# Optimization experiments

Measured on AMD Instinct MI355X. Metric: run time of the kernel, lower is better.

## Reference

```python
import jax, jax.numpy as jnp
import numpy as np

B, S, F, FFN = 8, 1024, 1024, 4096
F2 = FFN // 2          # NMF 'N' dim
R = 64                 # hamburger MD_R default
STEPS = 6              # number_of_iterations (TRAIN_STEPS == EVAL_STEPS)
EPS = 1e-6             # NMF2D denominator eps
LN_EPS = 1e-5


def setup_inputs() -> dict:
    key = jax.random.key(0)
    ks = jax.random.split(key, 6)
    x = jax.random.normal(ks[0], (B, S, F), jnp.float32)
    Wu = jax.random.normal(ks[1], (FFN, F), jnp.float32) / np.sqrt(F).astype(np.float32)
    bu = jnp.zeros((FFN,), jnp.float32)
    gamma = jnp.ones((F2,), jnp.float32)
    beta = jnp.zeros((F2,), jnp.float32)
    Wv = jax.random.normal(ks[2], (F, F2), jnp.float32) / np.sqrt(F2).astype(np.float32)
    bv = jnp.zeros((F,), jnp.float32)
    # NMF2D._build_bases: rand then F.normalize(dim=1) i.e. L2 over D(=seq) axis
    bases = jax.random.uniform(ks[3], (S, R), jnp.float32)
    bases = bases / jnp.linalg.norm(bases, axis=0, keepdims=True)
    return dict(x=x, Wu=Wu, bu=bu, gamma=gamma, beta=beta, Wv=Wv, bv=bv, bases=bases)


def _nmf_local_inference(xm, bas):
    # xm: (B, D, N) nonnegative, bas: (B, D, R)
    coef = jax.nn.softmax(jnp.einsum('bdn,bdr->bnr', xm, bas), axis=-1)  # inv_t = 1 for NMF2D

    def step(carry, _):
        bas, coef = carry
        # multiplicative update for coef (B, N, R)
        numer = jnp.einsum('bdn,bdr->bnr', xm, bas)
        denom = coef @ jnp.einsum('bdr,bds->brs', bas, bas)
        coef = coef * numer / (denom + EPS)
        # multiplicative update for bases (B, D, R)
        numer = jnp.einsum('bdn,bnr->bdr', xm, coef)
        denom = bas @ jnp.einsum('bnr,bns->brs', coef, coef)
        bas = bas * numer / (denom + EPS)
        return (bas, coef), None

    (bas, coef), _ = jax.lax.scan(step, (bas, coef), None, length=STEPS)
    return bas, coef


def reference(x, Wu, bu, gamma, beta, Wv, bv, bases):
    # gated MLP front: GELU(U(x)), chunk, ReLU(LN(z2))
    h = jax.nn.gelu(x @ Wu.T + bu, approximate=False)          # (B, S, FFN)
    z1, z2 = jnp.split(h, 2, axis=-1)                           # (B, S, F2) each
    mu = jnp.mean(z2, axis=-1, keepdims=True)
    var = jnp.mean((z2 - mu) ** 2, axis=-1, keepdims=True)
    z2 = (z2 - mu) / jnp.sqrt(var + LN_EPS) * gamma + beta
    z2 = jax.nn.relu(z2)

    # NMF2D: x viewed as (B, D=S, N=F2); bases buffer repeated over batch
    xm = z2                                                     # (B, D, N)
    bas0 = jnp.tile(bases[None], (B, 1, 1))                     # (B, D, R)
    # iterative solver runs under torch.no_grad in the original
    bas, coef = _nmf_local_inference(jax.lax.stop_gradient(xm), bas0)
    bas = jax.lax.stop_gradient(bas)
    coef = jax.lax.stop_gradient(coef)

    # compute_coef: one coef update WITH gradient through xm
    numer = jnp.einsum('bdn,bdr->bnr', xm, bas)
    denom = coef @ jnp.einsum('bdr,bds->brs', bas, bas)
    coef = coef * numer / (denom + EPS)

    z2r = jnp.einsum('bdr,bnr->bdn', bas, coef)                 # (B, S, F2) reconstruction

    out = (z1 * z2r) @ Wv.T + bv                                # (B, S, F)
    return out
```

## Files before the change

### kernel.cpp

```cpp
#include <hip/hip_runtime.h>
#include <math.h>

#define B_ 8
#define S_ 1024
#define F_ 1024
#define FFN_ 4096
#define F2_ 2048
#define R_ 64
#define NSTEPS 6
#define EPS_ 1e-6f
#define LN_EPS_ 1e-5f

typedef unsigned short u16;
typedef __attribute__((ext_vector_type(8))) short bf16x8;
typedef __attribute__((ext_vector_type(8))) unsigned short u16x8;
typedef __attribute__((ext_vector_type(4))) float f32x4;

__device__ __forceinline__ u16 f2bf(float f) {
    union { float f; unsigned int u; } c; c.f = f;
    unsigned int r = c.u + 0x7FFF + ((c.u >> 16) & 1);
    return (u16)(r >> 16);
}
__device__ __forceinline__ float bf2f(u16 u) {
    union { unsigned int u; float f; } c; c.u = ((unsigned int)u) << 16;
    return c.f;
}

__global__ __launch_bounds__(256) void k_cvt_bf16(const float* __restrict__ in,
        u16* __restrict__ out, int n8) {
    int i = blockIdx.x * 256 + threadIdx.x;
    if (i >= n8) return;
    const float4* p = (const float4*)in + (size_t)i * 2;
    float4 a = p[0], b = p[1];
    u16x8 o;
    o[0] = f2bf(a.x); o[1] = f2bf(a.y); o[2] = f2bf(a.z); o[3] = f2bf(a.w);
    o[4] = f2bf(b.x); o[5] = f2bf(b.y); o[6] = f2bf(b.z); o[7] = f2bf(b.w);
    *((u16x8*)out + i) = o;
}

template<int KD, int NOUT, bool GELUSPLIT>
__global__ __launch_bounds__(256) void k_mfma_bt(
        const u16* __restrict__ A, const u16* __restrict__ Bw,
        const float* __restrict__ bias,
        u16* __restrict__ obf, float* __restrict__ of1) {
    __shared__ u16 As[128 * 32];
    __shared__ u16 Bs[128 * 32];
    const int bm = blockIdx.x * 128;
    const int bn = blockIdx.y * 128;
    const int tid = threadIdx.x;
    const int wid = tid >> 6, lane = tid & 63;
    const int wr = wid >> 1, wc = wid & 1;
    const int lrow = lane & 15, lk = (lane >> 4) * 8;
    const int srow = lane >> 2, scol = (lane & 3) * 8;

    f32x4 acc[4][4] = {};

    const u16* Ag = A + (size_t)(bm + wid * 32) * KD;
    const u16* Bg = Bw + (size_t)(bn + wid * 32) * KD;

    for (int k0 = 0; k0 < KD; k0 += 32) {
        #pragma unroll
        for (int c = 0; c < 2; c++) {
            const u16* ga = Ag + (size_t)(c * 16 + srow) * KD + k0 + scol;
            u16* la = &As[(wid * 32 + c * 16) * 32];
            __builtin_amdgcn_global_load_lds(
                (const __attribute__((address_space(1))) void*)ga,
                (__attribute__((address_space(3))) void*)la, 16, 0, 0);
            const u16* gb = Bg + (size_t)(c * 16 + srow) * KD + k0 + scol;
            u16* lb = &Bs[(wid * 32 + c * 16) * 32];
            __builtin_amdgcn_global_load_lds(
                (const __attribute__((address_space(1))) void*)gb,
                (__attribute__((address_space(3))) void*)lb, 16, 0, 0);
        }
        __syncthreads();
        bf16x8 af[4], bfv[4];
        #pragma unroll
        for (int m = 0; m < 4; m++)
            af[m] = *(const bf16x8*)&As[(wr * 64 + m * 16 + lrow) * 32 + lk];
        #pragma unroll
        for (int n = 0; n < 4; n++)
            bfv[n] = *(const bf16x8*)&Bs[(wc * 64 + n * 16 + lrow) * 32 + lk];
        #pragma unroll
        for (int m = 0; m < 4; m++)
            #pragma unroll
            for (int n = 0; n < 4; n++)
                acc[m][n] = __builtin_amdgcn_mfma_f32_16x16x32_bf16(
                        af[m], bfv[n], acc[m][n], 0, 0, 0);
        __syncthreads();
    }

    const int crow = (lane >> 4) * 4;
    const int ccol = lane & 15;
    #pragma unroll
    for (int m = 0; m < 4; m++) {
        const int row = bm + wr * 64 + m * 16 + crow;
        #pragma unroll
        for (int n = 0; n < 4; n++) {
            const int col = bn + wc * 64 + n * 16 + ccol;
            const float bz = bias[col];
            #pragma unroll
            for (int r = 0; r < 4; r++) {
                float v = acc[m][n][r] + bz;
                if (GELUSPLIT) {
                    float g = 0.5f * v * (1.0f + erff(v * 0.7071067811865476f));
                    if (col < F2_) obf[(size_t)(row + r) * F2_ + col] = f2bf(g);
                    else           of1[(size_t)(row + r) * F2_ + (col - F2_)] = g;
                } else {
                    of1[(size_t)(row + r) * NOUT + col] = v;
                }
            }
        }
    }
}

template<int BM, int KD, int KCH, int M>
__global__ __launch_bounds__(256) void k_nmf_bt(
        const u16* __restrict__ A, const u16* __restrict__ Bw,
        float* __restrict__ outp) {
    __shared__ u16 As[BM * 32];
    __shared__ u16 Bs[64 * 32];
    constexpr int MR = BM / 32;
    const int bm = blockIdx.x * BM;
    const int ks = blockIdx.y;
    const int b  = blockIdx.z;
    const u16* Ab = A + (size_t)b * M * KD;
    const u16* Bb = Bw + (size_t)b * 64 * KD;
    const int tid = threadIdx.x;
    const int wid = tid >> 6, lane = tid & 63;
    const int wr = wid >> 1, wc = wid & 1;
    const int lrow = lane & 15, lk = (lane >> 4) * 8;
    const int srow = lane >> 2, scol = (lane & 3) * 8;

    f32x4 acc[MR][2] = {};
    const int kbeg = ks * (KD / KCH), kend = kbeg + KD / KCH;

    for (int k0 = kbeg; k0 < kend; k0 += 32) {
        #pragma unroll
        for (int c = 0; c < BM / 64; c++) {
            const int rowb = c * 64 + wid * 16;
            const u16* ga = Ab + (size_t)(bm + rowb + srow) * KD + k0 + scol;
            u16* la = &As[rowb * 32];
            __builtin_amdgcn_global_load_lds(
                (const __attribute__((address_space(1))) void*)ga,
                (__attribute__((address_space(3))) void*)la, 16, 0, 0);
        }
        {
            const int rowb = wid * 16;
            const u16* gb = Bb + (size_t)(rowb + srow) * KD + k0 + scol;
            u16* lb = &Bs[rowb * 32];
            __builtin_amdgcn_global_load_lds(
                (const __attribute__((address_space(1))) void*)gb,
                (__attribute__((address_space(3))) void*)lb, 16, 0, 0);
        }
        __syncthreads();
        bf16x8 af[MR], bf2[2];
        #pragma unroll
        for (int m = 0; m < MR; m++)
            af[m] = *(const bf16x8*)&As[(wr * (BM / 2) + m * 16 + lrow) * 32 + lk];
        #pragma unroll
        for (int n = 0; n < 2; n++)
            bf2[n] = *(const bf16x8*)&Bs[(wc * 32 + n * 16 + lrow) * 32 + lk];
        #pragma unroll
        for (int m = 0; m < MR; m++)
            #pragma unroll
            for (int n = 0; n < 2; n++)
                acc[m][n] = __builtin_amdgcn_mfma_f32_16x16x32_bf16(
                        af[m], bf2[n], acc[m][n], 0, 0, 0);
        __syncthreads();
    }

    const int crow = (lane >> 4) * 4;
    const int ccol = lane & 15;
    float* ob = outp + ((size_t)(ks * B_ + b) * M) * 64;
    #pragma unroll
    for (int m = 0; m < MR; m++) {
        const int row = bm + wr * (BM / 2) + m * 16 + crow;
        #pragma unroll
        for (int n = 0; n < 2; n++) {
            const int col = wc * 32 + n * 16 + ccol;
            #pragma unroll
            for (int r = 0; r < 4; r++)
                ob[(size_t)(row + r) * 64 + col] = acc[m][n][r];
        }
    }
}

__global__ __launch_bounds__(256) void k_ln_relu(const float* __restrict__ z2f,
        u16* __restrict__ xm_bf,
        const float* __restrict__ gamma, const float* __restrict__ beta) {
    const int row = blockIdx.x;
    const float* p = z2f + (size_t)row * F2_;
    const int i0 = threadIdx.x * 8;
    float4 a = *(const float4*)(p + i0);
    float4 b = *(const float4*)(p + i0 + 4);
    float v[8] = { a.x, a.y, a.z, a.w, b.x, b.y, b.z, b.w };
    float s = 0.f, sq = 0.f;
    #pragma unroll
    for (int j = 0; j < 8; j++) { s += v[j]; sq += v[j] * v[j]; }
    __shared__ float red0[4], red1[4];
    #pragma unroll
    for (int off = 32; off > 0; off >>= 1) {
        s  += __shfl_down(s, off);
        sq += __shfl_down(sq, off);
    }
    const int wid = threadIdx.x >> 6, lane = threadIdx.x & 63;
    if (lane == 0) { red0[wid] = s; red1[wid] = sq; }
    __syncthreads();
    if (threadIdx.x == 0) {
        float S = red0[0] + red0[1] + red0[2] + red0[3];
        float SQ = red1[0] + red1[1] + red1[2] + red1[3];
        float mu = S * (1.0f / F2_);
        float var = SQ * (1.0f / F2_) - mu * mu;
        red0[0] = mu;
        red1[0] = rsqrtf(var + LN_EPS_);
    }
    __syncthreads();
    const float mu = red0[0], inv = red1[0];
    u16x8 o;
    #pragma unroll
    for (int j = 0; j < 8; j++) {
        float w = (v[j] - mu) * inv * gamma[i0 + j] + beta[i0 + j];
        o[j] = f2bf(w > 0.f ? w : 0.f);
    }
    *(u16x8*)&xm_bf[(size_t)row * F2_ + i0] = o;
}

__global__ __launch_bounds__(256) void k_transpose_bf(const u16* __restrict__ in,
        u16* __restrict__ outp) {
    __shared__ u16 s[64][72];
    const int n0 = blockIdx.x * 64, d0 = blockIdx.y * 64, b = blockIdx.z;
    const u16* ib = in + (size_t)b * S_ * F2_;
    u16* ob = outp + (size_t)b * S_ * F2_;
    const int t = threadIdx.x;
    const int rr = t >> 3, cc = (t & 7) * 8;
    #pragma unroll
    for (int p = 0; p < 2; p++) {
        const int r = rr + p * 32;
        u16x8 v = *(const u16x8*)&ib[(size_t)(d0 + r) * F2_ + n0 + cc];
        #pragma unroll
        for (int j = 0; j < 8; j++) s[r][cc + j] = v[j];
    }
    __syncthreads();
    #pragma unroll
    for (int p = 0; p < 2; p++) {
        const int nr = rr + p * 32;
        u16x8 o;
        #pragma unroll
        for (int j = 0; j < 8; j++) o[j] = s[cc + j][nr];
        *(u16x8*)&ob[(size_t)(n0 + nr) * S_ + d0 + cc] = o;
    }
}

__global__ __launch_bounds__(256) void k_init_bases(const float* __restrict__ bases,
        float* __restrict__ bas, u16* __restrict__ basT) {
    const int i = blockIdx.x * 256 + threadIdx.x;
    const float v = bases[i];
    const int d = i >> 6, r = i & 63;
    const u16 vb = f2bf(v);
    #pragma unroll
    for (int b = 0; b < B_; b++) {
        bas[(size_t)b * S_ * R_ + i] = v;
        basT[(size_t)b * S_ * R_ + (size_t)r * S_ + d] = vb;
    }
}

__global__ __launch_bounds__(256) void k_softmax_coef(const float* __restrict__ ncp,
        float* __restrict__ coef, u16* __restrict__ coefT) {
    const size_t row = (size_t)blockIdx.x * 4 + (threadIdx.x >> 6);
    const int r = threadIdx.x & 63;
    const size_t CH = (size_t)B_ * F2_ * R_;
    float v = ncp[row * R_ + r] + ncp[CH + row * R_ + r];
    float m = v;
    #pragma unroll
    for (int off = 32; off > 0; off >>= 1) m = fmaxf(m, __shfl_xor(m, off));
    const float e = expf(v - m);
    float ssum = e;
    #pragma unroll
    for (int off = 32; off > 0; off >>= 1) ssum += __shfl_xor(ssum, off);
    const float cv = e / ssum;
    coef[row * R_ + r] = cv;
    const int b = (int)(row >> 11), n = (int)(row & 2047);
    coefT[((size_t)b * 64 + r) * F2_ + n] = f2bf(cv);
}

__global__ __launch_bounds__(256) void k_ata_part(const float* __restrict__ A,
        float* __restrict__ Gp, int K) {
    const int ks = blockIdx.x;
    const int b  = blockIdx.y;
    const int chunk = K >> 4;
    const float* Ab = A + ((size_t)b * K + (size_t)ks * chunk) * R_;
    __shared__ float As[16][68];
    const int tid = threadIdx.x, tx = tid & 15, ty = tid >> 4;
    float acc[4][4] = {};
    for (int k0 = 0; k0 < chunk; k0 += 16) {
        const int rr = tid & 63, q = tid >> 6;
        #pragma unroll
        for (int i = 0; i < 4; i++) {
            const int kk = q * 4 + i;
            As[kk][rr] = Ab[(size_t)(k0 + kk) * R_ + rr];
        }
        __syncthreads();
        #pragma unroll
        for (int kk = 0; kk < 16; kk++) {
            float a[4], bb[4];
            #pragma unroll
            for (int i = 0; i < 4; i++) a[i] = As[kk][ty * 4 + i];
            #pragma unroll
            for (int j = 0; j < 4; j++) bb[j] = As[kk][tx * 4 + j];
            #pragma unroll
            for (int i = 0; i < 4; i++)
                #pragma unroll
                for (int j = 0; j < 4; j++)
                    acc[i][j] = fmaf(a[i], bb[j], acc[i][j]);
        }
        __syncthreads();
    }
    #pragma unroll
    for (int i = 0; i < 4; i++)
        #pragma unroll
        for (int j = 0; j < 4; j++)
            Gp[(((size_t)b * 16 + ks) * R_ + ty * 4 + i) * R_ + tx * 4 + j] = acc[i][j];
}

__global__ __launch_bounds__(256) void k_ata_reduce(const float* __restrict__ Gp,
        float* __restrict__ G) {
    const int idx = blockIdx.x * 256 + threadIdx.x;
    const int b = idx >> 12, rs = idx & 4095;
    float s = 0.f;
    #pragma unroll
    for (int ks = 0; ks < 16; ks++) s += Gp[((size_t)b * 16 + ks) * 4096 + rs];
    G[idx] = s;
}

__global__ __launch_bounds__(256) void k_mult_update(float* __restrict__ M_,
        const float* __restrict__ numer_p, const float* __restrict__ G,
        int NR, size_t CH, u16* __restrict__ Tout, int TK) {
    const int b = blockIdx.y;
    const int row = blockIdx.x * 4 + (threadIdx.x >> 6);
    const int r = threadIdx.x & 63;
    __shared__ float Gs[64][68];
    __shared__ float Ms[4][64];
    const float* Gb = G + (size_t)b * R_ * R_;
    for (int i = threadIdx.x; i < 64 * 64; i += 256) Gs[i >> 6][i & 63] = Gb[i];
    const size_t base = ((size_t)b * NR + row) * R_;
    Ms[threadIdx.x >> 6][r] = M_[base + r];
    __syncthreads();
    float acc = 0.f;
    const int lrow = threadIdx.x >> 6;
    #pragma unroll
    for (int s = 0; s < 64; s++) acc = fmaf(Ms[lrow][s], Gs[s][r], acc);
    const float num = numer_p[base + r] + numer_p[CH + base + r];
    const float nv = Ms[lrow][r] * num / (acc + EPS_);
    M_[base + r] = nv;
    Tout[((size_t)b * 64 + r) * TK + row] = f2bf(nv);
}

__global__ __launch_bounds__(256) void k_recon_prod(const float* __restrict__ bas,
        const float* __restrict__ coef, u16* __restrict__ z1_bf) {
    const int d0 = blockIdx.x * 64;
    const int n0 = blockIdx.y * 64;
    const int b  = blockIdx.z;
    __shared__ float BasS[64][65], CoefS[64][65];
    const int tid = threadIdx.x, tx = tid & 15, ty = tid >> 4;
    {
        const int rr = tid & 63, q = tid >> 6;
        #pragma unroll
        for (int i = 0; i < 16; i++) {
            const int rowi = q * 16 + i;
            BasS[rowi][rr]  = bas[((size_t)b * S_ + d0 + rowi) * R_ + rr];
            CoefS[rowi][rr] = coef[((size_t)b * F2_ + n0 + rowi) * R_ + rr];
        }
    }
    __syncthreads();
    float acc[4][4] = {};
    #pragma unroll 8
    for (int r = 0; r < 64; r++) {
        float a[4], bb[4];
        #pragma unroll
        for (int i = 0; i < 4; i++) a[i] = BasS[ty * 4 + i][r];
        #pragma unroll
        for (int j = 0; j < 4; j++) bb[j] = CoefS[tx * 4 + j][r];
        #pragma unroll
        for (int i = 0; i < 4; i++)
            #pragma unroll
            for (int j = 0; j < 4; j++)
                acc[i][j] = fmaf(a[i], bb[j], acc[i][j]);
    }
    #pragma unroll
    for (int i = 0; i < 4; i++) {
        const size_t m = (size_t)b * S_ + d0 + ty * 4 + i;
        const size_t idx = m * F2_ + n0 + tx * 4;
        ushort4 zi = *(const ushort4*)&z1_bf[idx];
        ushort4 o;
        o.x = f2bf(bf2f(zi.x) * acc[i][0]);
        o.y = f2bf(bf2f(zi.y) * acc[i][1]);
        o.z = f2bf(bf2f(zi.z) * acc[i][2]);
        o.w = f2bf(bf2f(zi.w) * acc[i][3]);
        *(ushort4*)&z1_bf[idx] = o;
    }
}

extern "C" void kernel_launch(void* const* d_in, const int* in_sizes, int n_in,
                              void* d_out, int out_size, void* d_ws, size_t ws_size,
                              hipStream_t stream) {
    const float* x     = (const float*)d_in[0];
    const float* Wu    = (const float*)d_in[1];
    const float* bu    = (const float*)d_in[2];
    const float* gamma = (const float*)d_in[3];
    const float* beta  = (const float*)d_in[4];
    const float* Wv    = (const float*)d_in[5];
    const float* bv    = (const float*)d_in[6];
    const float* bases = (const float*)d_in[7];
    float* out = (float*)d_out;

    float* ws = (float*)d_ws;
    const size_t Z   = (size_t)B_ * S_ * F2_;
    const size_t NCR = (size_t)B_ * F2_ * R_;
    const size_t NBR = (size_t)B_ * S_ * R_;

    float* z2f    = ws;
    u16*   xmT_bf = (u16*)z2f;
    float* Gp     = z2f + Z / 2;
    float* G      = Gp + (size_t)16 * B_ * R_ * R_;
    float* p1 = z2f + Z;
    u16*   z1_bf  = (u16*)p1;
    float* p2 = p1 + Z / 2;
    u16*   xm_bf  = (u16*)p2;
    u16*   x_bf   = (u16*)p2;
    float* p3 = p2 + Z / 2;
    float* ncp    = p3;
    u16*   Wu_bf  = (u16*)p3;
    float* p4 = p3 + 2 * NCR;
    float* nbp    = p4;
    float* p5 = p4 + 2 * NBR;
    float* bas    = p5;
    float* p6 = p5 + NBR;
    u16*   basT_bf = (u16*)p6;
    float* p7 = p6 + NBR / 2;
    float* coef   = p7;
    u16*   Wv_bf  = (u16*)p7;
    float* p8 = p7 + NCR;
    u16*   coefT_bf = (u16*)p8;

    k_cvt_bf16<<<dim3(4096), 256, 0, stream>>>(x,  x_bf,  (int)((size_t)B_ * S_ * F_ / 8));
    k_cvt_bf16<<<dim3(2048), 256, 0, stream>>>(Wu, Wu_bf, (int)((size_t)FFN_ * F_ / 8));

    k_mfma_bt<F_, F2_, true><<<dim3(64, 32), 256, 0, stream>>>(x_bf, Wu_bf, bu, z1_bf, z2f);
    k_ln_relu<<<dim3(8192), 256, 0, stream>>>(z2f, xm_bf, gamma, beta);
    k_transpose_bf<<<dim3(32, 16, B_), 256, 0, stream>>>(xm_bf, xmT_bf);
    k_init_bases<<<dim3(256), 256, 0, stream>>>(bases, bas, basT_bf);

    k_nmf_bt<128, S_, 2, F2_><<<dim3(16, 2, B_), 256, 0, stream>>>(xmT_bf, basT_bf, ncp);
    k_softmax_coef<<<dim3(4096), 256, 0, stream>>>(ncp, coef, coefT_bf);

    for (int it = 0; it < NSTEPS; it++) {
        k_nmf_bt<128, S_, 2, F2_><<<dim3(16, 2, B_), 256, 0, stream>>>(xmT_bf, basT_bf, ncp);
        k_ata_part<<<dim3(16, B_), 256, 0, stream>>>(bas, Gp, S_);
        k_ata_reduce<<<dim3(128), 256, 0, stream>>>(Gp, G);
        k_mult_update<<<dim3(512, B_), 256, 0, stream>>>(coef, ncp, G, F2_, NCR, coefT_bf, F2_);
        k_nmf_bt<64, F2_, 2, S_><<<dim3(16, 2, B_), 256, 0, stream>>>(xm_bf, coefT_bf, nbp);
        k_ata_part<<<dim3(16, B_), 256, 0, stream>>>(coef, Gp, F2_);
        k_ata_reduce<<<dim3(128), 256, 0, stream>>>(Gp, G);
        k_mult_update<<<dim3(256, B_), 256, 0, stream>>>(bas, nbp, G, S_, NBR, basT_bf, S_);
    }

    k_nmf_bt<128, S_, 2, F2_><<<dim3(16, 2, B_), 256, 0, stream>>>(xmT_bf, basT_bf, ncp);
    k_ata_part<<<dim3(16, B_), 256, 0, stream>>>(bas, Gp, S_);
    k_ata_reduce<<<dim3(128), 256, 0, stream>>>(Gp, G);
    k_mult_update<<<dim3(512, B_), 256, 0, stream>>>(coef, ncp, G, F2_, NCR, coefT_bf, F2_);

    k_recon_prod<<<dim3(16, 32, B_), 256, 0, stream>>>(bas, coef, z1_bf);

    k_cvt_bf16<<<dim3(1024), 256, 0, stream>>>(Wv, Wv_bf, (int)((size_t)F_ * F2_ / 8));
    k_mfma_bt<F2_, F_, false><<<dim3(64, 8), 256, 0, stream>>>(z1_bf, Wv_bf, bv, nullptr, out);
}
```

Before: 812.3 us.

## Fuse Gram computation into NMF numerator kernel and store z2 as bf16

The separate two-kernel Gram computation (partial plus reduce) is folded into the NMF numerator GEMM launch as extra blocks, each computing a 64x16 slice of the Gram matrix directly. This removes two launches per update and the partial-sum round trip. The first iteration is peeled so the initial numerator launch can be reused by the first coef update. z2 is now written as bf16 instead of fp32 to halve the write and read traffic into LayerNorm, at some cost in LN statistic precision. The extra Gram blocks each scan the full K dimension serially, so they may become the tail of the launch.

```diff
diff --git a/kernel.cpp b/kernel.cpp
--- a/kernel.cpp
+++ b/kernel.cpp
@@ -42,7 +42,7 @@
 __global__ __launch_bounds__(256) void k_mfma_bt(
         const u16* __restrict__ A, const u16* __restrict__ Bw,
         const float* __restrict__ bias,
-        u16* __restrict__ obf, float* __restrict__ of1) {
+        u16* __restrict__ obf, u16* __restrict__ obf2, float* __restrict__ of1) {
     __shared__ u16 As[128 * 32];
     __shared__ u16 Bs[128 * 32];
     const int bm = blockIdx.x * 128;
@@ -104,7 +104,7 @@
                 if (GELUSPLIT) {
                     float g = 0.5f * v * (1.0f + erff(v * 0.7071067811865476f));
                     if (col < F2_) obf[(size_t)(row + r) * F2_ + col] = f2bf(g);
-                    else           of1[(size_t)(row + r) * F2_ + (col - F2_)] = g;
+                    else           obf2[(size_t)(row + r) * F2_ + (col - F2_)] = f2bf(g);
                 } else {
                     of1[(size_t)(row + r) * NOUT + col] = v;
                 }
@@ -113,87 +113,120 @@
     }
 }
 
-template<int BM, int KD, int KCH, int M>
-__global__ __launch_bounds__(256) void k_nmf_bt(
+template<int BM, int KD, int M, int AK>
+__global__ __launch_bounds__(256) void k_numer_gram(
         const u16* __restrict__ A, const u16* __restrict__ Bw,
-        float* __restrict__ outp) {
+        float* __restrict__ outp,
+        const float* __restrict__ Afp, float* __restrict__ G) {
     __shared__ u16 As[BM * 32];
     __shared__ u16 Bs[64 * 32];
-    constexpr int MR = BM / 32;
-    const int bm = blockIdx.x * BM;
-    const int ks = blockIdx.y;
-    const int b  = blockIdx.z;
-    const u16* Ab = A + (size_t)b * M * KD;
-    const u16* Bb = Bw + (size_t)b * 64 * KD;
+    __shared__ float Agr[16][65];
     const int tid = threadIdx.x;
-    const int wid = tid >> 6, lane = tid & 63;
-    const int wr = wid >> 1, wc = wid & 1;
-    const int lrow = lane & 15, lk = (lane >> 4) * 8;
-    const int srow = lane >> 2, scol = (lane & 3) * 8;
-
-    f32x4 acc[MR][2] = {};
-    const int kbeg = ks * (KD / KCH), kend = kbeg + KD / KCH;
-
-    for (int k0 = kbeg; k0 < kend; k0 += 32) {
-        #pragma unroll
-        for (int c = 0; c < BM / 64; c++) {
-            const int rowb = c * 64 + wid * 16;
-            const u16* ga = Ab + (size_t)(bm + rowb + srow) * KD + k0 + scol;
-            u16* la = &As[rowb * 32];
-            __builtin_amdgcn_global_load_lds(
-                (const __attribute__((address_space(1))) void*)ga,
-                (__attribute__((address_space(3))) void*)la, 16, 0, 0);
-        }
-        {
-            const int rowb = wid * 16;
-            const u16* gb = Bb + (size_t)(rowb + srow) * KD + k0 + scol;
-            u16* lb = &Bs[rowb * 32];
-            __builtin_amdgcn_global_load_lds(
-                (const __attribute__((address_space(1))) void*)gb,
-                (__attribute__((address_space(3))) void*)lb, 16, 0, 0);
-        }
-        __syncthreads();
-        bf16x8 af[MR], bf2[2];
-        #pragma unroll
-        for (int m = 0; m < MR; m++)
-            af[m] = *(const bf16x8*)&As[(wr * (BM / 2) + m * 16 + lrow) * 32 + lk];
-        #pragma unroll
-        for (int n = 0; n < 2; n++)
-            bf2[n] = *(const bf16x8*)&Bs[(wc * 32 + n * 16 + lrow) * 32 + lk];
-        #pragma unroll
-        for (int m = 0; m < MR; m++)
+    const int b = blockIdx.z;
+
+    if (blockIdx.x < 16) {
+        constexpr int MR = BM / 32;
+        const int bm = blockIdx.x * BM;
+        const int ks = blockIdx.y;
+        const u16* Ab = A + (size_t)b * M * KD;
+        const u16* Bb = Bw + (size_t)b * 64 * KD;
+        const int wid = tid >> 6, lane = tid & 63;
+        const int wr = wid >> 1, wc = wid & 1;
+        const int lrow = lane & 15, lk = (lane >> 4) * 8;
+        const int srow = lane >> 2, scol = (lane & 3) * 8;
+
+        f32x4 acc[MR][2] = {};
+        const int kbeg = ks * (KD / 2), kend = kbeg + KD / 2;
+
+        for (int k0 = kbeg; k0 < kend; k0 += 32) {
+            #pragma unroll
+            for (int c = 0; c < BM / 64; c++) {
+                const int rowb = c * 64 + wid * 16;
+                const u16* ga = Ab + (size_t)(bm + rowb + srow) * KD + k0 + scol;
+                u16* la = &As[rowb * 32];
+                __builtin_amdgcn_global_load_lds(
+                    (const __attribute__((address_space(1))) void*)ga,
+                    (__attribute__((address_space(3))) void*)la, 16, 0, 0);
+            }
+            {
+                const int rowb = wid * 16;
+                const u16* gb = Bb + (size_t)(rowb + srow) * KD + k0 + scol;
+                u16* lb = &Bs[rowb * 32];
+                __builtin_amdgcn_global_load_lds(
+                    (const __attribute__((address_space(1))) void*)gb,
+                    (__attribute__((address_space(3))) void*)lb, 16, 0, 0);
+            }
+            __syncthreads();
+            bf16x8 af[MR], bf2[2];
+            #pragma unroll
+            for (int m = 0; m < MR; m++)
+                af[m] = *(const bf16x8*)&As[(wr * (BM / 2) + m * 16 + lrow) * 32 + lk];
             #pragma unroll
             for (int n = 0; n < 2; n++)
-                acc[m][n] = __builtin_amdgcn_mfma_f32_16x16x32_bf16(
-                        af[m], bf2[n], acc[m][n], 0, 0, 0);
-        __syncthreads();
-    }
-
-    const int crow = (lane >> 4) * 4;
-    const int ccol = lane & 15;
-    float* ob = outp + ((size_t)(ks * B_ + b) * M) * 64;
-    #pragma unroll
-    for (int m = 0; m < MR; m++) {
-        const int row = bm + wr * (BM / 2) + m * 16 + crow;
-        #pragma unroll
-        for (int n = 0; n < 2; n++) {
-            const int col = wc * 32 + n * 16 + ccol;
-            #pragma unroll
-            for (int r = 0; r < 4; r++)
-                ob[(size_t)(row + r) * 64 + col] = acc[m][n][r];
-        }
-    }
-}
-
-__global__ __launch_bounds__(256) void k_ln_relu(const float* __restrict__ z2f,
+                bf2[n] = *(const bf16x8*)&Bs[(wc * 32 + n * 16 + lrow) * 32 + lk];
+            #pragma unroll
+            for (int m = 0; m < MR; m++)
+                #pragma unroll
+                for (int n = 0; n < 2; n++)
+                    acc[m][n] = __builtin_amdgcn_mfma_f32_16x16x32_bf16(
+                            af[m], bf2[n], acc[m][n], 0, 0, 0);
+            __syncthreads();
+        }
+
+        const int crow = (lane >> 4) * 4;
+        const int ccol = lane & 15;
+        float* ob = outp + ((size_t)(ks * B_ + b) * M) * 64;
+        #pragma unroll
+        for (int m = 0; m < MR; m++) {
+            const int row = bm + wr * (BM / 2) + m * 16 + crow;
+            #pragma unroll
+            for (int n = 0; n < 2; n++) {
+                const int col = wc * 32 + n * 16 + ccol;
+                #pragma unroll
+                for (int r = 0; r < 4; r++)
+                    ob[(size_t)(row + r) * 64 + col] = acc[m][n][r];
+            }
+        }
+    } else {
+        const int schunk = (blockIdx.x - 16) * 2 + blockIdx.y;
+        const int s0 = schunk * 16;
+        const float* Ab = Afp + (size_t)b * AK * 64;
+        const int r = tid & 63;
+        const int sg = tid >> 6;
+        float acc[4] = {};
+        for (int k0 = 0; k0 < AK; k0 += 16) {
+            #pragma unroll
+            for (int i = 0; i < 4; i++) {
+                const int idx = tid + i * 256;
+                Agr[idx >> 6][idx & 63] = Ab[(size_t)(k0 + (idx >> 6)) * 64 + (idx & 63)];
+            }
+            __syncthreads();
+            #pragma unroll
+            for (int kk = 0; kk < 16; kk++) {
+                const float ar = Agr[kk][r];
+                #pragma unroll
+                for (int j = 0; j < 4; j++)
+                    acc[j] = fmaf(ar, Agr[kk][s0 + sg * 4 + j], acc[j]);
+            }
+            __syncthreads();
+        }
+        float* Gb = G + (size_t)b * R_ * R_;
+        #pragma unroll
+        for (int j = 0; j < 4; j++)
+            Gb[(size_t)r * R_ + s0 + sg * 4 + j] = acc[j];
+    }
+}
+
+__global__ __launch_bounds__(256) void k_ln_relu(const u16* __restrict__ z2bf,
         u16* __restrict__ xm_bf,
         const float* __restrict__ gamma, const float* __restrict__ beta) {
     const int row = blockIdx.x;
-    const float* p = z2f + (size_t)row * F2_;
+    const u16* p = z2bf + (size_t)row * F2_;
     const int i0 = threadIdx.x * 8;
-    float4 a = *(const float4*)(p + i0);
-    float4 b = *(const float4*)(p + i0 + 4);
-    float v[8] = { a.x, a.y, a.z, a.w, b.x, b.y, b.z, b.w };
+    u16x8 a = *(const u16x8*)(p + i0);
+    float v[8];
+    #pragma unroll
+    for (int j = 0; j < 8; j++) v[j] = bf2f(a[j]);
     float s = 0.f, sq = 0.f;
     #pragma unroll
     for (int j = 0; j < 8; j++) { s += v[j]; sq += v[j] * v[j]; }
@@ -281,55 +314,6 @@
     coef[row * R_ + r] = cv;
     const int b = (int)(row >> 11), n = (int)(row & 2047);
     coefT[((size_t)b * 64 + r) * F2_ + n] = f2bf(cv);
-}
-
-__global__ __launch_bounds__(256) void k_ata_part(const float* __restrict__ A,
-        float* __restrict__ Gp, int K) {
-    const int ks = blockIdx.x;
-    const int b  = blockIdx.y;
-    const int chunk = K >> 4;
-    const float* Ab = A + ((size_t)b * K + (size_t)ks * chunk) * R_;
-    __shared__ float As[16][68];
-    const int tid = threadIdx.x, tx = tid & 15, ty = tid >> 4;
-    float acc[4][4] = {};
-    for (int k0 = 0; k0 < chunk; k0 += 16) {
-        const int rr = tid & 63, q = tid >> 6;
-        #pragma unroll
-        for (int i = 0; i < 4; i++) {
-            const int kk = q * 4 + i;
-            As[kk][rr] = Ab[(size_t)(k0 + kk) * R_ + rr];
-        }
-        __syncthreads();
-        #pragma unroll
-        for (int kk = 0; kk < 16; kk++) {
-            float a[4], bb[4];
-            #pragma unroll
-            for (int i = 0; i < 4; i++) a[i] = As[kk][ty * 4 + i];
-            #pragma unroll
-            for (int j = 0; j < 4; j++) bb[j] = As[kk][tx * 4 + j];
-            #pragma unroll
-            for (int i = 0; i < 4; i++)
-                #pragma unroll
-                for (int j = 0; j < 4; j++)
-                    acc[i][j] = fmaf(a[i], bb[j], acc[i][j]);
-        }
-        __syncthreads();
-    }
-    #pragma unroll
-    for (int i = 0; i < 4; i++)
-        #pragma unroll
-        for (int j = 0; j < 4; j++)
-            Gp[(((size_t)b * 16 + ks) * R_ + ty * 4 + i) * R_ + tx * 4 + j] = acc[i][j];
-}
-
-__global__ __launch_bounds__(256) void k_ata_reduce(const float* __restrict__ Gp,
-        float* __restrict__ G) {
-    const int idx = blockIdx.x * 256 + threadIdx.x;
-    const int b = idx >> 12, rs = idx & 4095;
-    float s = 0.f;
-    #pragma unroll
-    for (int ks = 0; ks < 16; ks++) s += Gp[((size_t)b * 16 + ks) * 4096 + rs];
-    G[idx] = s;
 }
 
 __global__ __launch_bounds__(256) void k_mult_update(float* __restrict__ M_,
@@ -417,60 +401,52 @@
     const size_t Z   = (size_t)B_ * S_ * F2_;
     const size_t NCR = (size_t)B_ * F2_ * R_;
     const size_t NBR = (size_t)B_ * S_ * R_;
-
-    float* z2f    = ws;
-    u16*   xmT_bf = (u16*)z2f;
-    float* Gp     = z2f + Z / 2;
-    float* G      = Gp + (size_t)16 * B_ * R_ * R_;
-    float* p1 = z2f + Z;
-    u16*   z1_bf  = (u16*)p1;
-    float* p2 = p1 + Z / 2;
-    u16*   xm_bf  = (u16*)p2;
-    u16*   x_bf   = (u16*)p2;
-    float* p3 = p2 + Z / 2;
-    float* ncp    = p3;
-    u16*   Wu_bf  = (u16*)p3;
-    float* p4 = p3 + 2 * NCR;
-    float* nbp    = p4;
-    float* p5 = p4 + 2 * NBR;
-    float* bas    = p5;
-    float* p6 = p5 + NBR;
-    u16*   basT_bf = (u16*)p6;
-    float* p7 = p6 + NBR / 2;
-    float* coef   = p7;
-    u16*   Wv_bf  = (u16*)p7;
-    float* p8 = p7 + NCR;
-    u16*   coefT_bf = (u16*)p8;
-
-    k_cvt_bf16<<<dim3(4096), 256, 0, stream>>>(x,  x_bf,  (int)((size_t)B_ * S_ * F_ / 8));
-    k_cvt_bf16<<<dim3(2048), 256, 0, stream>>>(Wu, Wu_bf, (int)((size_t)FFN_ * F_ / 8));
-
-    k_mfma_bt<F_, F2_, true><<<dim3(64, 32), 256, 0, stream>>>(x_bf, Wu_bf, bu, z1_bf, z2f);
-    k_ln_relu<<<dim3(8192), 256, 0, stream>>>(z2f, xm_bf, gamma, beta);
+    const size_t XBF = (size_t)B_ * S_ * F_;
+    const size_t WUBF = (size_t)FFN_ * F_;
+
+    u16*   x_bf   = (u16*)ws;
+    u16*   Wu_bf  = x_bf + XBF;
+    u16*   z2_bf  = Wu_bf + WUBF;
+    u16*   xmT_bf = (u16*)ws;
+    float* G      = (float*)((u16*)ws + Z);
+    u16*   Wv_bf  = (u16*)(G + (size_t)B_ * R_ * R_);
+    float* p = ws + (Z + XBF + WUBF) / 2;
+    u16*   z1_bf  = (u16*)p;               p += Z / 2;
+    u16*   xm_bf  = (u16*)p;               p += Z / 2;
+    float* ncp    = p;                     p += 2 * NCR;
+    float* nbp    = p;                     p += 2 * NBR;
+    float* bas    = p;                     p += NBR;
+    u16*   basT_bf = (u16*)p;              p += NBR / 2;
+    float* coef   = p;                     p += NCR;
+    u16*   coefT_bf = (u16*)p;
+
+    k_cvt_bf16<<<dim3(4096), 256, 0, stream>>>(x,  x_bf,  (int)(XBF / 8));
+    k_cvt_bf16<<<dim3(2048), 256, 0, stream>>>(Wu, Wu_bf, (int)(WUBF / 8));
+
+    k_mfma_bt<F_, F2_, true><<<dim3(64, 32), 256, 0, stream>>>(x_bf, Wu_bf, bu, z1_bf, z2_bf, nullptr);
+    k_ln_relu<<<dim3(8192), 256, 0, stream>>>(z2_bf, xm_bf, gamma, beta);
     k_transpose_bf<<<dim3(32, 16, B_), 256, 0, stream>>>(xm_bf, xmT_bf);
     k_init_bases<<<dim3(256), 256, 0, stream>>>(bases, bas, basT_bf);
 
-    k_nmf_bt<128, S_, 2, F2_><<<dim3(16, 2, B_), 256, 0, stream>>>(xmT_bf, basT_bf, ncp);
+    k_numer_gram<128, S_, F2_, S_><<<dim3(18, 2, B_), 256, 0, stream>>>(xmT_bf, basT_bf, ncp, bas, G);
     k_softmax_coef<<<dim3(4096), 256, 0, stream>>>(ncp, coef, coefT_bf);
 
-    for (int it = 0; it < NSTEPS; it++) {
-        k_nmf_bt<128, S_, 2, F2_><<<dim3(16, 2, B_), 256, 0, stream>>>(xmT_bf, basT_bf, ncp);
-        k_ata_part<<<dim3(16, B_), 256, 0, stream>>>(bas, Gp, S_);
-        k_ata_reduce<<<dim3(128), 256, 0, stream>>>(Gp, G);
+    k_mult_update<<<dim3(512, B_), 256, 0, stream>>>(coef, ncp, G, F2_, NCR, coefT_bf, F2_);
+    k_numer_gram<64, F2_, S_, F2_><<<dim3(18, 2, B_), 256, 0, stream>>>(xm_bf, coefT_bf, nbp, coef, G);
+    k_mult_update<<<dim3(256, B_), 256, 0, stream>>>(bas, nbp, G, S_, NBR, basT_bf, S_);
+
+    for (int it = 1; it < NSTEPS; it++) {
+        k_numer_gram<128, S_, F2_, S_><<<dim3(18, 2, B_), 256, 0, stream>>>(xmT_bf, basT_bf, ncp, bas, G);
         k_mult_update<<<dim3(512, B_), 256, 0, stream>>>(coef, ncp, G, F2_, NCR, coefT_bf, F2_);
-        k_nmf_bt<64, F2_, 2, S_><<<dim3(16, 2, B_), 256, 0, stream>>>(xm_bf, coefT_bf, nbp);
-        k_ata_part<<<dim3(16, B_), 256, 0, stream>>>(coef, Gp, F2_);
-        k_ata_reduce<<<dim3(128), 256, 0, stream>>>(Gp, G);
+        k_numer_gram<64, F2_, S_, F2_><<<dim3(18, 2, B_), 256, 0, stream>>>(xm_bf, coefT_bf, nbp, coef, G);
         k_mult_update<<<dim3(256, B_), 256, 0, stream>>>(bas, nbp, G, S_, NBR, basT_bf, S_);
     }
 
-    k_nmf_bt<128, S_, 2, F2_><<<dim3(16, 2, B_), 256, 0, stream>>>(xmT_bf, basT_bf, ncp);
-    k_ata_part<<<dim3(16, B_), 256, 0, stream>>>(bas, Gp, S_);
-    k_ata_reduce<<<dim3(128), 256, 0, stream>>>(Gp, G);
+    k_numer_gram<128, S_, F2_, S_><<<dim3(18, 2, B_), 256, 0, stream>>>(xmT_bf, basT_bf, ncp, bas, G);
     k_mult_update<<<dim3(512, B_), 256, 0, stream>>>(coef, ncp, G, F2_, NCR, coefT_bf, F2_);
 
     k_recon_prod<<<dim3(16, 32, B_), 256, 0, stream>>>(bas, coef, z1_bf);
 
     k_cvt_bf16<<<dim3(1024), 256, 0, stream>>>(Wv, Wv_bf, (int)((size_t)F_ * F2_ / 8));
-    k_mfma_bt<F2_, F_, false><<<dim3(64, 8), 256, 0, stream>>>(z1_bf, Wv_bf, bv, nullptr, out);
-}
+    k_mfma_bt<F2_, F_, false><<<dim3(64, 8), 256, 0, stream>>>(z1_bf, Wv_bf, bv, nullptr, nullptr, out);
+}
```

Measured after the change: 1.330 ms. +63.7%, slower.

## Store z2 as bf16, split NMF GEMMs 4-way, reuse initial numerator

Applied to the files above, without the earlier changes.

The GELU GEMM now writes the LayerNorm input half as bf16 instead of fp32, halving that round trip. NMF projection GEMMs use 4-way split-K instead of 2-way, doubling block count for better occupancy at the cost of more partial-sum traffic. The first solver iteration is peeled to reuse the numerator already computed for the softmax initialisation, removing one redundant GEMM. Storing z2 in bf16 slightly reduces LayerNorm input precision.

```diff
diff --git a/kernel.cpp b/kernel.cpp
--- a/kernel.cpp
+++ b/kernel.cpp
@@ -42,7 +42,7 @@
 __global__ __launch_bounds__(256) void k_mfma_bt(
         const u16* __restrict__ A, const u16* __restrict__ Bw,
         const float* __restrict__ bias,
-        u16* __restrict__ obf, float* __restrict__ of1) {
+        u16* __restrict__ obf, u16* __restrict__ obf2, float* __restrict__ of1) {
     __shared__ u16 As[128 * 32];
     __shared__ u16 Bs[128 * 32];
     const int bm = blockIdx.x * 128;
@@ -104,7 +104,7 @@
                 if (GELUSPLIT) {
                     float g = 0.5f * v * (1.0f + erff(v * 0.7071067811865476f));
                     if (col < F2_) obf[(size_t)(row + r) * F2_ + col] = f2bf(g);
-                    else           of1[(size_t)(row + r) * F2_ + (col - F2_)] = g;
+                    else           obf2[(size_t)(row + r) * F2_ + (col - F2_)] = f2bf(g);
                 } else {
                     of1[(size_t)(row + r) * NOUT + col] = v;
                 }
@@ -185,15 +185,16 @@
     }
 }
 
-__global__ __launch_bounds__(256) void k_ln_relu(const float* __restrict__ z2f,
+__global__ __launch_bounds__(256) void k_ln_relu(const u16* __restrict__ z2bf,
         u16* __restrict__ xm_bf,
         const float* __restrict__ gamma, const float* __restrict__ beta) {
     const int row = blockIdx.x;
-    const float* p = z2f + (size_t)row * F2_;
+    const u16* p = z2bf + (size_t)row * F2_;
     const int i0 = threadIdx.x * 8;
-    float4 a = *(const float4*)(p + i0);
-    float4 b = *(const float4*)(p + i0 + 4);
-    float v[8] = { a.x, a.y, a.z, a.w, b.x, b.y, b.z, b.w };
+    u16x8 a = *(const u16x8*)(p + i0);
+    float v[8];
+    #pragma unroll
+    for (int j = 0; j < 8; j++) v[j] = bf2f(a[j]);
     float s = 0.f, sq = 0.f;
     #pragma unroll
     for (int j = 0; j < 8; j++) { s += v[j]; sq += v[j] * v[j]; }
@@ -269,7 +270,9 @@
     const size_t row = (size_t)blockIdx.x * 4 + (threadIdx.x >> 6);
     const int r = threadIdx.x & 63;
     const size_t CH = (size_t)B_ * F2_ * R_;
-    float v = ncp[row * R_ + r] + ncp[CH + row * R_ + r];
+    float v = 0.f;
+    #pragma unroll
+    for (int c = 0; c < 4; c++) v += ncp[c * CH + row * R_ + r];
     float m = v;
     #pragma unroll
     for (int off = 32; off > 0; off >>= 1) m = fmaxf(m, __shfl_xor(m, off));
@@ -349,7 +352,9 @@
     const int lrow = threadIdx.x >> 6;
     #pragma unroll
     for (int s = 0; s < 64; s++) acc = fmaf(Ms[lrow][s], Gs[s][r], acc);
-    const float num = numer_p[base + r] + numer_p[CH + base + r];
+    float num = 0.f;
+    #pragma unroll
+    for (int c = 0; c < 4; c++) num += numer_p[c * CH + base + r];
     const float nv = Ms[lrow][r] * num / (acc + EPS_);
     M_[base + r] = nv;
     Tout[((size_t)b * 64 + r) * TK + row] = f2bf(nv);
@@ -417,54 +422,57 @@
     const size_t Z   = (size_t)B_ * S_ * F2_;
     const size_t NCR = (size_t)B_ * F2_ * R_;
     const size_t NBR = (size_t)B_ * S_ * R_;
-
-    float* z2f    = ws;
-    u16*   xmT_bf = (u16*)z2f;
-    float* Gp     = z2f + Z / 2;
-    float* G      = Gp + (size_t)16 * B_ * R_ * R_;
-    float* p1 = z2f + Z;
-    u16*   z1_bf  = (u16*)p1;
-    float* p2 = p1 + Z / 2;
-    u16*   xm_bf  = (u16*)p2;
-    u16*   x_bf   = (u16*)p2;
-    float* p3 = p2 + Z / 2;
-    float* ncp    = p3;
-    u16*   Wu_bf  = (u16*)p3;
-    float* p4 = p3 + 2 * NCR;
-    float* nbp    = p4;
-    float* p5 = p4 + 2 * NBR;
-    float* bas    = p5;
-    float* p6 = p5 + NBR;
-    u16*   basT_bf = (u16*)p6;
-    float* p7 = p6 + NBR / 2;
-    float* coef   = p7;
-    u16*   Wv_bf  = (u16*)p7;
-    float* p8 = p7 + NCR;
-    u16*   coefT_bf = (u16*)p8;
-
-    k_cvt_bf16<<<dim3(4096), 256, 0, stream>>>(x,  x_bf,  (int)((size_t)B_ * S_ * F_ / 8));
-    k_cvt_bf16<<<dim3(2048), 256, 0, stream>>>(Wu, Wu_bf, (int)((size_t)FFN_ * F_ / 8));
-
-    k_mfma_bt<F_, F2_, true><<<dim3(64, 32), 256, 0, stream>>>(x_bf, Wu_bf, bu, z1_bf, z2f);
-    k_ln_relu<<<dim3(8192), 256, 0, stream>>>(z2f, xm_bf, gamma, beta);
+    const size_t XBF = (size_t)B_ * S_ * F_;
+    const size_t WUBF = (size_t)FFN_ * F_;
+
+    u16*   x_bf   = (u16*)ws;
+    u16*   Wu_bf  = x_bf + XBF;
+    u16*   z2_bf  = Wu_bf + WUBF;
+    u16*   xmT_bf = (u16*)ws;
+    float* G      = (float*)((u16*)ws + Z);
+    float* Gp     = G + (size_t)B_ * R_ * R_;
+    u16*   Wv_bf  = (u16*)(Gp + (size_t)16 * B_ * R_ * R_);
+    float* p = ws + (Z + XBF + WUBF) / 2;
+    u16*   z1_bf  = (u16*)p;               p += Z / 2;
+    u16*   xm_bf  = (u16*)p;               p += Z / 2;
+    float* ncp    = p;                     p += 4 * NCR;
+    float* nbp    = p;                     p += 4 * NBR;
+    float* bas    = p;                     p += NBR;
+    u16*   basT_bf = (u16*)p;              p += NBR / 2;
+    float* coef   = p;                     p += NCR;
+    u16*   coefT_bf = (u16*)p;
+
+    k_cvt_bf16<<<dim3(4096), 256, 0, stream>>>(x,  x_bf,  (int)(XBF / 8));
+    k_cvt_bf16<<<dim3(2048), 256, 0, stream>>>(Wu, Wu_bf, (int)(WUBF / 8));
+
+    k_mfma_bt<F_, F2_, true><<<dim3(64, 32), 256, 0, stream>>>(x_bf, Wu_bf, bu, z1_bf, z2_bf, nullptr);
+    k_ln_relu<<<dim3(8192), 256, 0, stream>>>(z2_bf, xm_bf, gamma, beta);
     k_transpose_bf<<<dim3(32, 16, B_), 256, 0, stream>>>(xm_bf, xmT_bf);
     k_init_bases<<<dim3(256), 256, 0, stream>>>(bases, bas, basT_bf);
 
-    k_nmf_bt<128, S_, 2, F2_><<<dim3(16, 2, B_), 256, 0, stream>>>(xmT_bf, basT_bf, ncp);
+    k_nmf_bt<128, S_, 4, F2_><<<dim3(16, 4, B_), 256, 0, stream>>>(xmT_bf, basT_bf, ncp);
+    k_ata_part<<<dim3(16, B_), 256, 0, stream>>>(bas, Gp, S_);
+    k_ata_reduce<<<dim3(128), 256, 0, stream>>>(Gp, G);
     k_softmax_coef<<<dim3(4096), 256, 0, stream>>>(ncp, coef, coefT_bf);
 
-    for (int it = 0; it < NSTEPS; it++) {
-        k_nmf_bt<128, S_, 2, F2_><<<dim3(16, 2, B_), 256, 0, stream>>>(xmT_bf, basT_bf, ncp);
+    k_mult_update<<<dim3(512, B_), 256, 0, stream>>>(coef, ncp, G, F2_, NCR, coefT_bf, F2_);
+    k_nmf_bt<64, F2_, 4, S_><<<dim3(16, 4, B_), 256, 0, stream>>>(xm_bf, coefT_bf, nbp);
+    k_ata_part<<<dim3(16, B_), 256, 0, stream>>>(coef, Gp, F2_);
+    k_ata_reduce<<<dim3(128), 256, 0, stream>>>(Gp, G);
+    k_mult_update<<<dim3(256, B_), 256, 0, stream>>>(bas, nbp, G, S_, NBR, basT_bf, S_);
+
+    for (int it = 1; it < NSTEPS; it++) {
+        k_nmf_bt<128, S_, 4, F2_><<<dim3(16, 4, B_), 256, 0, stream>>>(xmT_bf, basT_bf, ncp);
         k_ata_part<<<dim3(16, B_), 256, 0, stream>>>(bas, Gp, S_);
         k_ata_reduce<<<dim3(128), 256, 0, stream>>>(Gp, G);
         k_mult_update<<<dim3(512, B_), 256, 0, stream>>>(coef, ncp, G, F2_, NCR, coefT_bf, F2_);
-        k_nmf_bt<64, F2_, 2, S_><<<dim3(16, 2, B_), 256, 0, stream>>>(xm_bf, coefT_bf, nbp);
+        k_nmf_bt<64, F2_, 4, S_><<<dim3(16, 4, B_), 256, 0, stream>>>(xm_bf, coefT_bf, nbp);
         k_ata_part<<<dim3(16, B_), 256, 0, stream>>>(coef, Gp, F2_);
         k_ata_reduce<<<dim3(128), 256, 0, stream>>>(Gp, G);
         k_mult_update<<<dim3(256, B_), 256, 0, stream>>>(bas, nbp, G, S_, NBR, basT_bf, S_);
     }
 
-    k_nmf_bt<128, S_, 2, F2_><<<dim3(16, 2, B_), 256, 0, stream>>>(xmT_bf, basT_bf, ncp);
+    k_nmf_bt<128, S_, 4, F2_><<<dim3(16, 4, B_), 256, 0, stream>>>(xmT_bf, basT_bf, ncp);
     k_ata_part<<<dim3(16, B_), 256, 0, stream>>>(bas, Gp, S_);
     k_ata_reduce<<<dim3(128), 256, 0, stream>>>(Gp, G);
     k_mult_update<<<dim3(512, B_), 256, 0, stream>>>(coef, ncp, G, F2_, NCR, coefT_bf, F2_);
@@ -472,5 +480,5 @@
     k_recon_prod<<<dim3(16, 32, B_), 256, 0, stream>>>(bas, coef, z1_bf);
 
     k_cvt_bf16<<<dim3(1024), 256, 0, stream>>>(Wv, Wv_bf, (int)((size_t)F_ * F2_ / 8));
-    k_mfma_bt<F2_, F_, false><<<dim3(64, 8), 256, 0, stream>>>(z1_bf, Wv_bf, bv, nullptr, out);
-}
+    k_mfma_bt<F2_, F_, false><<<dim3(64, 8), 256, 0, stream>>>(z1_bf, Wv_bf, bv, nullptr, nullptr, out);
+}
```

Measured after the change: 774.8 us. -4.6%, faster.
